# Performance work log

Hardware: AMD Instinct MI355X
Metric: run time of the kernel (lower is better)

Reference implementation:

```python
import jax, jax.numpy as jnp
import numpy as np

N = 100000      # rows of edge_features / scatter dim_size
E = 1000000     # edges
C_IN = 16
C_OUT = 16
H = 32
DIM = 3
RADIUS = 1.0
EPS = 1e-5


def setup_inputs() -> dict:
    key = jax.random.key(0)
    ks = jax.random.split(key, 8)
    s1 = 1.0 / np.sqrt(DIM)
    s2 = 1.0 / np.sqrt(H)
    return {
        "in_edges": jax.random.randint(ks[0], (E,), 0, N, dtype=jnp.int32),
        "out_edges": jax.random.randint(ks[1], (E,), 0, N, dtype=jnp.int32),
        "edge_features": jax.random.normal(ks[2], (N, C_IN), dtype=jnp.float32),
        "hood_coords": jax.random.normal(ks[3], (E, DIM), dtype=jnp.float32),
        "W1": jax.random.normal(ks[4], (DIM, H), dtype=jnp.float32) * s1,
        "b1": jnp.zeros((H,), jnp.float32),
        "g1": jnp.ones((H,), jnp.float32),
        "beta1": jnp.zeros((H,), jnp.float32),
        "W2": jax.random.normal(ks[5], (H, H), dtype=jnp.float32) * s2,
        "b2": jnp.zeros((H,), jnp.float32),
        "g2": jnp.ones((H,), jnp.float32),
        "beta2": jnp.zeros((H,), jnp.float32),
        "W3": jax.random.normal(ks[6], (H, C_IN * C_OUT), dtype=jnp.float32) * s2,
        "b3": jnp.zeros((C_IN * C_OUT,), jnp.float32),
    }


def _layernorm(x, g, b):
    m = jnp.mean(x, axis=-1, keepdims=True)
    v = jnp.mean((x - m) ** 2, axis=-1, keepdims=True)
    return (x - m) * jax.lax.rsqrt(v + EPS) * g + b


def reference(in_edges, out_edges, edge_features, hood_coords,
              W1, b1, g1, beta1, W2, b2, g2, beta2, W3, b3):
    # neural field: coords -> per-edge weight matrix [E, C_OUT, C_IN]
    x = hood_coords / RADIUS
    x = jax.nn.relu(_layernorm(x @ W1 + b1, g1, beta1))
    x = jax.nn.relu(_layernorm(x @ W2 + b2, g2, beta2))
    w = jnp.tanh(x @ W3 + b3).reshape(-1, C_OUT, C_IN)
    # gather + per-edge matvec
    f = edge_features[in_edges]                      # [E, C_IN]
    out_ch = jnp.einsum('ni,noi->no', f, w)          # [E, C_OUT]
    # scatter_mean over out_edges with dim_size = N
    sums = jax.ops.segment_sum(out_ch, out_edges, num_segments=N)
    counts = jax.ops.segment_sum(jnp.ones((out_ch.shape[0],), out_ch.dtype),
                                 out_edges, num_segments=N)
    return sums / jnp.maximum(counts, 1.0)[:, None]
```

## Files before the change

kernel.cpp:

```cpp
#include <hip/hip_runtime.h>
#include <hip/hip_bf16.h>


typedef __attribute__((ext_vector_type(4)))  short    short4v;
typedef __attribute__((ext_vector_type(4)))  float    float4v;
typedef __attribute__((ext_vector_type(16))) float    f32x16;
typedef __attribute__((ext_vector_type(4)))  unsigned uint4v;
typedef __attribute__((ext_vector_type(2)))  unsigned uint2v;

constexpr float LN_EPS   = 1e-5f;
constexpr float LOG2E_X2 = 2.8853900817779268f;

__device__ __forceinline__ unsigned f2bf(float x) {
  unsigned u = __builtin_bit_cast(unsigned, x);
  u += 0x7FFFu + ((u >> 16) & 1u);
  return u >> 16;
}
__device__ __forceinline__ unsigned pack2(float lo, float hi) {
  return f2bf(lo) | (f2bf(hi) << 16);
}
__device__ __forceinline__ unsigned packc(float lo, float hi) {
  float2 v; v.x = lo; v.y = hi;
  const __hip_bfloat162 b = __float22bfloat162_rn(v);
  static_assert(sizeof(__hip_bfloat162) == 4, "bf16x2 must be 4 bytes");
  unsigned r;
  __builtin_memcpy(&r, &b, 4);
  return r;
}
__device__ __forceinline__ float bflo2f(unsigned u) {
  return __builtin_bit_cast(float, u << 16);
}
__device__ __forceinline__ float bfhi2f(unsigned u) {
  return __builtin_bit_cast(float, u & 0xFFFF0000u);
}
__device__ __forceinline__ float sigm2(float x) {
  return __builtin_amdgcn_rcpf(__builtin_amdgcn_exp2f(x) + 1.0f);
}

__device__ __forceinline__ f32x16 mfma32(short4v a, short4v b, f32x16 c) {
#if __has_builtin(__builtin_amdgcn_mfma_f32_32x32x8bf16_1k)
  return __builtin_amdgcn_mfma_f32_32x32x8bf16_1k(a, b, c, 0, 0, 0);
#else
  asm volatile("v_mfma_f32_32x32x8_bf16 %0, %1, %2, %0\n\ts_nop 7\n\ts_nop 7"
               : "+v"(c) : "v"(a), "v"(b));
  return c;
#endif
}

__device__ __forceinline__ void ln_relu_pack32f(const float* hv,
                                                const float* __restrict__ gf,
                                                const float* __restrict__ bef,
                                                short4v* bh) {
  float sum = 0.f, ss = 0.f;
#pragma unroll
  for (int i = 0; i < 16; ++i) { sum += hv[i]; ss += hv[i] * hv[i]; }
  sum += __shfl_xor(sum, 32);
  ss  += __shfl_xor(ss, 32);
  const float m   = sum * (1.0f / 32.0f);
  const float var = fmaxf(ss * (1.0f / 32.0f) - m * m, 0.f);
  const float rs  = rsqrtf(var + LN_EPS);
#pragma unroll
  for (int s = 0; s < 4; ++s) {
    const float4v gv = *(const float4v*)&gf[s * 4];
    const float4v bv = *(const float4v*)&bef[s * 4];
    float y[4];
#pragma unroll
    for (int j = 0; j < 4; ++j)
      y[j] = fmaxf((hv[s * 4 + j] - m) * rs * gv[j] + bv[j], 0.f);
    uint2v u; u[0] = packc(y[0], y[1]); u[1] = packc(y[2], y[3]);
    bh[s] = __builtin_bit_cast(short4v, u);
  }
}


__global__ void nf_hist(const int* __restrict__ out_edges, int* __restrict__ counts, int E) {
  const int t4 = (blockIdx.x * blockDim.x + threadIdx.x) * 4;
  if (t4 + 3 < E) {
    const int4 v = *(const int4*)(out_edges + t4);
    atomicAdd(&counts[v.x], 1);
    atomicAdd(&counts[v.y], 1);
    atomicAdd(&counts[v.z], 1);
    atomicAdd(&counts[v.w], 1);
  } else {
    for (int i = t4; i < E; ++i) atomicAdd(&counts[out_edges[i]], 1);
  }
}

__global__ void nf_alloc(const int* __restrict__ counts, int* __restrict__ offsets,
                         int* __restrict__ cursor, int* __restrict__ total, int N) {
  const int i = blockIdx.x * blockDim.x + threadIdx.x;
  const int lane = threadIdx.x & 63;
  int c = (i < N) ? counts[i] : 0;
  int sc = c;
#pragma unroll
  for (int d = 1; d < 64; d <<= 1) {
    int v = __shfl_up(sc, d);
    if (lane >= d) sc += v;
  }
  const int excl = sc - c;
  const int wtot = __shfl(sc, 63);
  int base = 0;
  if (lane == 0) base = atomicAdd(total, wtot);
  base = __shfl(base, 0);
  if (i < N) {
    offsets[i] = base + excl;
    cursor[i]  = base + excl;
  }
}


template <int SCATTER_MODE>
__global__ __launch_bounds__(256, 2)
void nf_main(const int* __restrict__ in_edges,
             const int* __restrict__ out_edges,
             const float* __restrict__ ef,
             const float* __restrict__ coords,
             const float* __restrict__ W1, const float* __restrict__ b1,
             const float* __restrict__ g1, const float* __restrict__ be1,
             const float* __restrict__ W2, const float* __restrict__ b2,
             const float* __restrict__ g2, const float* __restrict__ be2,
             const float* __restrict__ W3, const float* __restrict__ b3,
             void* __restrict__ out_ch,
             int* __restrict__ aux,
             int* __restrict__ cursor,
             int E, int ntiles)
{
  __shared__ __align__(16) unsigned sA3[8 * 2 * 64 * 4];
  __shared__ __align__(16) float    sB3f[256];
  __shared__ __align__(16) float    sB2f[2][16];
  __shared__ __align__(16) float    sB1f[2][16];
  __shared__ __align__(16) float    sG1[2][16],  sBe1[2][16];
  __shared__ __align__(16) float    sG2[2][16],  sBe2[2][16];

  const int t    = threadIdx.x;
  const int l    = t & 63;
  const int h    = l >> 5;
  const int ecol = l & 31;

#pragma unroll
  for (int rep = 0; rep < 16; ++rep) {
    const int idx = rep * 256 + t;
    const int u = idx & 3, ll = (idx >> 2) & 63, b = (idx >> 8) & 1, mt = idx >> 9;
    const int s = b * 2 + (u >> 1), jp = u & 1;
    const int hh = ll >> 5, m = ll & 31;
    const int o = 2 * mt + (m >> 4), i = m & 15;
    const int k0 = 8 * s + 4 * hh + 2 * jp;
    sA3[idx] = pack2(LOG2E_X2 * W3[(size_t)k0 * 256 + o * 16 + i],
                     LOG2E_X2 * W3[(size_t)(k0 + 1) * 256 + o * 16 + i]);
  }
  sB3f[t] = LOG2E_X2 * b3[t];
  if (t < 32) {
    const int hh = t >> 4, r = t & 15;
    const int ch = 8 * (r >> 2) + 4 * hh + (r & 3);
    sB2f[hh][r] = b2[ch];
    sB1f[hh][r] = b1[ch];
    sG1[hh][r]  = g1[ch];   sBe1[hh][r] = be1[ch];
    sG2[hh][r]  = g2[ch];   sBe2[hh][r] = be2[ch];
  }

  short4v a1;
#pragma unroll
  for (int j = 0; j < 4; ++j) {
    const int k = 4 * h + j;
    a1[j] = (k < 3) ? (short)f2bf(W1[k * 32 + ecol]) : (short)0;
  }
  short4v a2[4];
#pragma unroll
  for (int s = 0; s < 4; ++s) {
    short4v v;
#pragma unroll
    for (int j = 0; j < 4; ++j)
      v[j] = (short)f2bf(W2[(8 * s + 4 * h + j) * 32 + ecol]);
    a2[s] = v;
  }
  __syncthreads();

  const int gwave  = (blockIdx.x * blockDim.x + t) >> 6;
  const int nwaves = (gridDim.x * blockDim.x) >> 6;

  int tile = gwave;
  bool valid = false; int oe = 0;
  float x0 = 0.f, x1 = 0.f, x2 = 0.f;
  float4v f4a = {}, f4b = {};
  if (tile < ntiles) {
    const int eIdx = tile * 32 + ecol;
    valid = eIdx < E;
    const int eS = valid ? eIdx : 0;
    const int ie = in_edges[eS]; oe = out_edges[eS];
    x0 = coords[3 * eS]; x1 = coords[3 * eS + 1]; x2 = coords[3 * eS + 2];
    f4a = *(const float4v*)(ef + (size_t)ie * 16 + 4 * h);
    f4b = *(const float4v*)(ef + (size_t)ie * 16 + 8 + 4 * h);
  }

  for (; tile < ntiles; tile += nwaves) {
    const int tn = tile + nwaves;
    int ieN = 0, oeN = 0; bool validN = false;
    float x0N = 0.f, x1N = 0.f, x2N = 0.f;
    if (tn < ntiles) {
      const int eIdxN = tn * 32 + ecol;
      validN = eIdxN < E;
      const int eSN = validN ? eIdxN : 0;
      ieN = in_edges[eSN]; oeN = out_edges[eSN];
      x0N = coords[3 * eSN]; x1N = coords[3 * eSN + 1]; x2N = coords[3 * eSN + 2];
    }

    int pos = 0;
    if (SCATTER_MODE == 0 && h == 0 && valid)
      pos = atomicAdd(&cursor[oe], 1);

    short4v bx;
    {
      uint2v u;
      u[0] = h ? 0u : packc(x0, x1);
      u[1] = h ? 0u : packc(x2, 0.f);
      bx = __builtin_bit_cast(short4v, u);
    }
    f32x16 c;
    {
      const float4v* bb = (const float4v*)&sB1f[h][0];
      const float4v i0 = bb[0], i1 = bb[1], i2 = bb[2], i3 = bb[3];
#pragma unroll
      for (int e = 0; e < 4; ++e) {
        c[e] = i0[e]; c[4 + e] = i1[e]; c[8 + e] = i2[e]; c[12 + e] = i3[e];
      }
    }
    c = mfma32(a1, bx, c);

    float hv[16];
#pragma unroll
    for (int r = 0; r < 16; ++r) hv[r] = c[r];
    short4v bh[4];
    ln_relu_pack32f(hv, &sG1[h][0], &sBe1[h][0], bh);

    {
      const float4v* bb = (const float4v*)&sB2f[h][0];
      const float4v i0 = bb[0], i1 = bb[1], i2 = bb[2], i3 = bb[3];
#pragma unroll
      for (int e = 0; e < 4; ++e) {
        c[e] = i0[e]; c[4 + e] = i1[e]; c[8 + e] = i2[e]; c[12 + e] = i3[e];
      }
    }
#pragma unroll
    for (int s = 0; s < 4; ++s) c = mfma32(a2[s], bh[s], c);

#pragma unroll
    for (int r = 0; r < 16; ++r) hv[r] = c[r];
    ln_relu_pack32f(hv, &sG2[h][0], &sBe2[h][0], bh);

    float4v f4aN = {}, f4bN = {};
    if (tn < ntiles) {
      f4aN = *(const float4v*)(ef + (size_t)ieN * 16 + 4 * h);
      f4bN = *(const float4v*)(ef + (size_t)ieN * 16 + 8 + 4 * h);
    }

    const float sumf = (f4a[0] + f4a[1]) + (f4a[2] + f4a[3])
                     + (f4b[0] + f4b[1]) + (f4b[2] + f4b[3]);

#pragma unroll 1
    for (int mt = 0; mt < 8; ++mt) {
      const uint4v av0 = *(const uint4v*)&sA3[mt * 512 + (l << 2)];
      const uint4v av1 = *(const uint4v*)&sA3[mt * 512 + 256 + (l << 2)];
      f32x16 c3;
      {
        const float4v i0 = *(const float4v*)&sB3f[(2 * mt) * 16 + 4 * h];
        const float4v i1 = *(const float4v*)&sB3f[(2 * mt) * 16 + 8 + 4 * h];
        const float4v i2 = *(const float4v*)&sB3f[(2 * mt + 1) * 16 + 4 * h];
        const float4v i3 = *(const float4v*)&sB3f[(2 * mt + 1) * 16 + 8 + 4 * h];
#pragma unroll
        for (int e = 0; e < 4; ++e) {
          c3[e] = i0[e]; c3[4 + e] = i1[e]; c3[8 + e] = i2[e]; c3[12 + e] = i3[e];
        }
      }
      uint2v u01, u23;
      u01[0] = av0[0]; u01[1] = av0[1];  u23[0] = av0[2]; u23[1] = av0[3];
      c3 = mfma32(__builtin_bit_cast(short4v, u01), bh[0], c3);
      c3 = mfma32(__builtin_bit_cast(short4v, u23), bh[1], c3);
      u01[0] = av1[0]; u01[1] = av1[1];  u23[0] = av1[2]; u23[1] = av1[3];
      c3 = mfma32(__builtin_bit_cast(short4v, u01), bh[2], c3);
      c3 = mfma32(__builtin_bit_cast(short4v, u23), bh[3], c3);

      float dot0 = 0.f, dot1 = 0.f;
#pragma unroll
      for (int j = 0; j < 4; ++j) {
        dot0 = fmaf(f4a[j], sigm2(c3[j]),      dot0);
        dot0 = fmaf(f4b[j], sigm2(c3[4 + j]),  dot0);
        dot1 = fmaf(f4a[j], sigm2(c3[8 + j]),  dot1);
        dot1 = fmaf(f4b[j], sigm2(c3[12 + j]), dot1);
      }
      float pr0 = fmaf(-2.0f, dot0, sumf);
      float pr1 = fmaf(-2.0f, dot1, sumf);
      pr0 += __shfl_xor(pr0, 32);
      pr1 += __shfl_xor(pr1, 32);

      if (SCATTER_MODE == 0) {
        if (h == 0 && valid)
          ((unsigned*)out_ch)[(size_t)pos * 8 + mt] = packc(pr0, pr1);
      } else {
        if (h == 0 && valid) {
          float* sums = (float*)out_ch;
          atomicAdd(&sums[(size_t)oe * 16 + 2 * mt],     pr0);
          atomicAdd(&sums[(size_t)oe * 16 + 2 * mt + 1], pr1);
        }
      }
    }
    if (SCATTER_MODE == 1) {
      if (h == 0 && valid) atomicAdd(&aux[oe], 1);
    }

    valid = validN; oe = oeN;
    x0 = x0N; x1 = x1N; x2 = x2N; f4a = f4aN; f4b = f4bN;
  }
}


__global__ __launch_bounds__(256)
void nf_reduce(const uint4v* __restrict__ out_chb4, const int* __restrict__ counts,
               const int* __restrict__ offsets, float* __restrict__ out, int N) {
  const int gid  = blockIdx.x * 128 + (threadIdx.x >> 1);
  const int half = threadIdx.x & 1;
  if (gid >= N) return;
  const int deg = counts[gid];
  const int off = offsets[gid];
  float a[8] = {0.f, 0.f, 0.f, 0.f, 0.f, 0.f, 0.f, 0.f};
  for (int d = 0; d < deg; ++d) {
    const uint4v u = out_chb4[(size_t)(off + d) * 2 + half];
#pragma unroll
    for (int p = 0; p < 4; ++p) {
      a[2 * p]     += bflo2f(u[p]);
      a[2 * p + 1] += bfhi2f(u[p]);
    }
  }
  const float inv = 1.0f / fmaxf((float)deg, 1.0f);
  float4v r0, r1;
#pragma unroll
  for (int p = 0; p < 4; ++p) { r0[p] = a[p] * inv; r1[p] = a[4 + p] * inv; }
  float* dst = out + (size_t)gid * 16 + 8 * half;
  *(float4v*)dst       = r0;
  *(float4v*)(dst + 4) = r1;
}

__global__ void nf_final(float* __restrict__ out, const int* __restrict__ counts, int n) {
  int i = blockIdx.x * blockDim.x + threadIdx.x;
  if (i < n) {
    float c = (float)counts[i >> 4];
    out[i] = out[i] / fmaxf(c, 1.0f);
  }
}

extern "C" void kernel_launch(void* const* d_in, const int* in_sizes, int n_in,
                              void* d_out, int out_size, void* d_ws, size_t ws_size,
                              hipStream_t stream) {
  const int*   in_edges  = (const int*)d_in[0];
  const int*   out_edges = (const int*)d_in[1];
  const float* ef        = (const float*)d_in[2];
  const float* coords    = (const float*)d_in[3];
  const float* W1  = (const float*)d_in[4];
  const float* b1  = (const float*)d_in[5];
  const float* g1  = (const float*)d_in[6];
  const float* be1 = (const float*)d_in[7];
  const float* W2  = (const float*)d_in[8];
  const float* b2  = (const float*)d_in[9];
  const float* g2  = (const float*)d_in[10];
  const float* be2 = (const float*)d_in[11];
  const float* W3  = (const float*)d_in[12];
  const float* b3  = (const float*)d_in[13];

  const int E = in_sizes[0];
  const int N = in_sizes[2] / 16;
  const int ntiles = (E + 31) / 32;
  float* out = (float*)d_out;

  const size_t need = ((size_t)E * 8 + 3 * (size_t)N + 1) * 4;

  if (ws_size >= need) {
    unsigned* out_chb = (unsigned*)d_ws;
    int*      counts  = (int*)(out_chb + (size_t)E * 8);
    int*      total   = counts + N;
    int*      offsets = total + 1;
    int*      cursor  = offsets + N;

    (void)hipMemsetAsync(counts, 0, ((size_t)N + 1) * sizeof(int), stream);
    nf_hist<<<(E / 4 + 255) / 256 + 1, 256, 0, stream>>>(out_edges, counts, E);
    nf_alloc<<<(N + 255) / 256, 256, 0, stream>>>(counts, offsets, cursor, total, N);
    nf_main<0><<<1536, 256, 0, stream>>>(in_edges, out_edges, ef, coords,
                                         W1, b1, g1, be1, W2, b2, g2, be2, W3, b3,
                                         out_chb, nullptr, cursor, E, ntiles);
    nf_reduce<<<(N + 127) / 128, 256, 0, stream>>>((const uint4v*)out_chb, counts,
                                                   offsets, out, N);
  } else {
    int* counts = (int*)d_ws;
    (void)hipMemsetAsync(out, 0, (size_t)out_size * sizeof(float), stream);
    (void)hipMemsetAsync(counts, 0, (size_t)N * sizeof(int), stream);
    nf_main<1><<<1536, 256, 0, stream>>>(in_edges, out_edges, ef, coords,
                                         W1, b1, g1, be1, W2, b2, g2, be2, W3, b3,
                                         out, counts, nullptr, E, ntiles);
    nf_final<<<(out_size + 255) / 256, 256, 0, stream>>>(out, counts, out_size);
  }
}
```

Baseline: 176.6 us.

## Software-pipeline the MLP front stages one tile ahead with deeper index prefetch

```diff
diff --git a/kernel.cpp b/kernel.cpp
--- a/kernel.cpp
+++ b/kernel.cpp
@@ -175,39 +175,7 @@
   }
   __syncthreads();
 
-  const int gwave  = (blockIdx.x * blockDim.x + t) >> 6;
-  const int nwaves = (gridDim.x * blockDim.x) >> 6;
-
-  int tile = gwave;
-  bool valid = false; int oe = 0;
-  float x0 = 0.f, x1 = 0.f, x2 = 0.f;
-  float4v f4a = {}, f4b = {};
-  if (tile < ntiles) {
-    const int eIdx = tile * 32 + ecol;
-    valid = eIdx < E;
-    const int eS = valid ? eIdx : 0;
-    const int ie = in_edges[eS]; oe = out_edges[eS];
-    x0 = coords[3 * eS]; x1 = coords[3 * eS + 1]; x2 = coords[3 * eS + 2];
-    f4a = *(const float4v*)(ef + (size_t)ie * 16 + 4 * h);
-    f4b = *(const float4v*)(ef + (size_t)ie * 16 + 8 + 4 * h);
-  }
-
-  for (; tile < ntiles; tile += nwaves) {
-    const int tn = tile + nwaves;
-    int ieN = 0, oeN = 0; bool validN = false;
-    float x0N = 0.f, x1N = 0.f, x2N = 0.f;
-    if (tn < ntiles) {
-      const int eIdxN = tn * 32 + ecol;
-      validN = eIdxN < E;
-      const int eSN = validN ? eIdxN : 0;
-      ieN = in_edges[eSN]; oeN = out_edges[eSN];
-      x0N = coords[3 * eSN]; x1N = coords[3 * eSN + 1]; x2N = coords[3 * eSN + 2];
-    }
-
-    int pos = 0;
-    if (SCATTER_MODE == 0 && h == 0 && valid)
-      pos = atomicAdd(&cursor[oe], 1);
-
+  auto front = [&](float x0, float x1, float x2, short4v* bh) {
     short4v bx;
     {
       uint2v u;
@@ -229,7 +197,6 @@
     float hv[16];
 #pragma unroll
     for (int r = 0; r < 16; ++r) hv[r] = c[r];
-    short4v bh[4];
     ln_relu_pack32f(hv, &sG1[h][0], &sBe1[h][0], bh);
 
     {
@@ -246,6 +213,39 @@
 #pragma unroll
     for (int r = 0; r < 16; ++r) hv[r] = c[r];
     ln_relu_pack32f(hv, &sG2[h][0], &sBe2[h][0], bh);
+  };
+
+  const int gwave  = (blockIdx.x * blockDim.x + t) >> 6;
+  const int nwaves = (gridDim.x * blockDim.x) >> 6;
+
+  int tile = gwave;
+  bool validC = false; int oeC = 0;
+  short4v bhC[4] = {};
+  float4v f4aC = {}, f4bC = {};
+  bool validN = false; int ieN = 0, oeN = 0;
+  float xN0 = 0.f, xN1 = 0.f, xN2 = 0.f;
+
+  if (tile < ntiles) {
+    const int eIdx = tile * 32 + ecol;
+    validC = eIdx < E;
+    const int eS = validC ? eIdx : 0;
+    const int ie = in_edges[eS]; oeC = out_edges[eS];
+    const float x0 = coords[3 * eS], x1 = coords[3 * eS + 1], x2 = coords[3 * eS + 2];
+    f4aC = *(const float4v*)(ef + (size_t)ie * 16 + 4 * h);
+    f4bC = *(const float4v*)(ef + (size_t)ie * 16 + 8 + 4 * h);
+    front(x0, x1, x2, bhC);
+  }
+  if (tile + nwaves < ntiles) {
+    const int eIdx = (tile + nwaves) * 32 + ecol;
+    validN = eIdx < E;
+    const int eS = validN ? eIdx : 0;
+    ieN = in_edges[eS]; oeN = out_edges[eS];
+    xN0 = coords[3 * eS]; xN1 = coords[3 * eS + 1]; xN2 = coords[3 * eS + 2];
+  }
+
+  for (; tile < ntiles; tile += nwaves) {
+    const int tn  = tile + nwaves;
+    const int tnn = tile + 2 * nwaves;
 
     float4v f4aN = {}, f4bN = {};
     if (tn < ntiles) {
@@ -253,8 +253,26 @@
       f4bN = *(const float4v*)(ef + (size_t)ieN * 16 + 8 + 4 * h);
     }
 
-    const float sumf = (f4a[0] + f4a[1]) + (f4a[2] + f4a[3])
-                     + (f4b[0] + f4b[1]) + (f4b[2] + f4b[3]);
+    int pos = 0;
+    if (SCATTER_MODE == 0 && h == 0 && validC)
+      pos = atomicAdd(&cursor[oeC], 1);
+
+    bool validNN = false; int ieNN = 0, oeNN = 0;
+    float xNN0 = 0.f, xNN1 = 0.f, xNN2 = 0.f;
+    if (tnn < ntiles) {
+      const int eIdx = tnn * 32 + ecol;
+      validNN = eIdx < E;
+      const int eS = validNN ? eIdx : 0;
+      ieNN = in_edges[eS]; oeNN = out_edges[eS];
+      xNN0 = coords[3 * eS]; xNN1 = coords[3 * eS + 1]; xNN2 = coords[3 * eS + 2];
+    }
+
+    short4v bhN[4] = {};
+    if (tn < ntiles)
+      front(xN0, xN1, xN2, bhN);
+
+    const float sumf = (f4aC[0] + f4aC[1]) + (f4aC[2] + f4aC[3])
+                     + (f4bC[0] + f4bC[1]) + (f4bC[2] + f4bC[3]);
 
 #pragma unroll 1
     for (int mt = 0; mt < 8; ++mt) {
@@ -273,19 +291,19 @@
       }
       uint2v u01, u23;
       u01[0] = av0[0]; u01[1] = av0[1];  u23[0] = av0[2]; u23[1] = av0[3];
-      c3 = mfma32(__builtin_bit_cast(short4v, u01), bh[0], c3);
-      c3 = mfma32(__builtin_bit_cast(short4v, u23), bh[1], c3);
+      c3 = mfma32(__builtin_bit_cast(short4v, u01), bhC[0], c3);
+      c3 = mfma32(__builtin_bit_cast(short4v, u23), bhC[1], c3);
       u01[0] = av1[0]; u01[1] = av1[1];  u23[0] = av1[2]; u23[1] = av1[3];
-      c3 = mfma32(__builtin_bit_cast(short4v, u01), bh[2], c3);
-      c3 = mfma32(__builtin_bit_cast(short4v, u23), bh[3], c3);
+      c3 = mfma32(__builtin_bit_cast(short4v, u01), bhC[2], c3);
+      c3 = mfma32(__builtin_bit_cast(short4v, u23), bhC[3], c3);
 
       float dot0 = 0.f, dot1 = 0.f;
 #pragma unroll
       for (int j = 0; j < 4; ++j) {
-        dot0 = fmaf(f4a[j], sigm2(c3[j]),      dot0);
-        dot0 = fmaf(f4b[j], sigm2(c3[4 + j]),  dot0);
-        dot1 = fmaf(f4a[j], sigm2(c3[8 + j]),  dot1);
-        dot1 = fmaf(f4b[j], sigm2(c3[12 + j]), dot1);
+        dot0 = fmaf(f4aC[j], sigm2(c3[j]),      dot0);
+        dot0 = fmaf(f4bC[j], sigm2(c3[4 + j]),  dot0);
+        dot1 = fmaf(f4aC[j], sigm2(c3[8 + j]),  dot1);
+        dot1 = fmaf(f4bC[j], sigm2(c3[12 + j]), dot1);
       }
       float pr0 = fmaf(-2.0f, dot0, sumf);
       float pr1 = fmaf(-2.0f, dot1, sumf);
@@ -293,22 +311,24 @@
       pr1 += __shfl_xor(pr1, 32);
 
       if (SCATTER_MODE == 0) {
-        if (h == 0 && valid)
+        if (h == 0 && validC)
           ((unsigned*)out_ch)[(size_t)pos * 8 + mt] = packc(pr0, pr1);
       } else {
-        if (h == 0 && valid) {
+        if (h == 0 && validC) {
           float* sums = (float*)out_ch;
-          atomicAdd(&sums[(size_t)oe * 16 + 2 * mt],     pr0);
-          atomicAdd(&sums[(size_t)oe * 16 + 2 * mt + 1], pr1);
+          atomicAdd(&sums[(size_t)oeC * 16 + 2 * mt],     pr0);
+          atomicAdd(&sums[(size_t)oeC * 16 + 2 * mt + 1], pr1);
         }
       }
     }
     if (SCATTER_MODE == 1) {
-      if (h == 0 && valid) atomicAdd(&aux[oe], 1);
-    }
-
-    valid = validN; oe = oeN;
-    x0 = x0N; x1 = x1N; x2 = x2N; f4a = f4aN; f4b = f4bN;
+      if (h == 0 && validC) atomicAdd(&aux[oeC], 1);
+    }
+
+    bhC[0] = bhN[0]; bhC[1] = bhN[1]; bhC[2] = bhN[2]; bhC[3] = bhN[3];
+    f4aC = f4aN; f4bC = f4bN; oeC = oeN; validC = validN;
+    ieN = ieNN; oeN = oeNN; validN = validNN;
+    xN0 = xNN0; xN1 = xNN1; xN2 = xNN2;
   }
 }
 
```

Result: faster. 172.1 us (-2.6%).
